# Optimization experiments

Measured on AMD Instinct MI355X. Metric: run time of the kernel, lower is better.

Reference implementation:

```python
import jax, jax.numpy as jnp
import numpy as np

N_NODES = 100000
N_EDGES = 1000000
NUM_FEATURES = 64
HIDDEN = 64
NUM_GRAPHS = 128


def setup_inputs() -> dict:
    key = jax.random.key(0)
    ks = jax.random.split(key, 12)
    x = jax.random.normal(ks[0], (N_NODES, NUM_FEATURES), dtype=jnp.float32)
    edge_index = jax.random.randint(ks[1], (2, N_EDGES), 0, N_NODES, dtype=jnp.int64)
    edge_weight = jax.random.uniform(ks[2], (N_EDGES,), dtype=jnp.float32)
    batch = jnp.sort(jax.random.randint(ks[3], (N_NODES,), 0, NUM_GRAPHS, dtype=jnp.int64))
    s1 = 1.0 / np.sqrt(NUM_FEATURES)
    s2 = 1.0 / np.sqrt(HIDDEN)
    # GraphConv layer 1: lin_rel (with bias) applied to aggregated msgs, lin_root (no bias)
    w1_rel = jax.random.uniform(ks[4], (HIDDEN, NUM_FEATURES), jnp.float32, -s1, s1)
    b1_rel = jax.random.uniform(ks[5], (HIDDEN,), jnp.float32, -s1, s1)
    w1_root = jax.random.uniform(ks[6], (HIDDEN, NUM_FEATURES), jnp.float32, -s1, s1)
    # GraphConv layer 2
    w2_rel = jax.random.uniform(ks[7], (HIDDEN, HIDDEN), jnp.float32, -s2, s2)
    b2_rel = jax.random.uniform(ks[8], (HIDDEN,), jnp.float32, -s2, s2)
    w2_root = jax.random.uniform(ks[9], (HIDDEN, HIDDEN), jnp.float32, -s2, s2)
    # final Linear(hidden, 1)
    w_lin = jax.random.uniform(ks[10], (1, HIDDEN), jnp.float32, -s2, s2)
    b_lin = jax.random.uniform(ks[11], (1,), jnp.float32, -s2, s2)
    return {
        "x": x, "edge_index": edge_index, "edge_weight": edge_weight, "batch": batch,
        "w1_rel": w1_rel, "b1_rel": b1_rel, "w1_root": w1_root,
        "w2_rel": w2_rel, "b2_rel": b2_rel, "w2_root": w2_root,
        "w_lin": w_lin, "b_lin": b_lin,
    }


def graph_conv(x, edge_index, edge_weight, w_rel, b_rel, w_root):
    # messages: x[src] * e, scatter-add into dst  (gather-scale-scatter)
    src, dst = edge_index[0], edge_index[1]
    msgs = x[src] * edge_weight[:, None]                      # [E, F]
    aggr = jax.ops.segment_sum(msgs, dst, num_segments=x.shape[0])  # [N, F]
    return aggr @ w_rel.T + b_rel + x @ w_root.T


def reference(x, edge_index, edge_weight, batch,
              w1_rel, b1_rel, w1_root, w2_rel, b2_rel, w2_root, w_lin, b_lin):
    h = graph_conv(x, edge_index, edge_weight, w1_rel, b1_rel, w1_root)
    h = jax.nn.relu(h)
    h = graph_conv(h, edge_index, edge_weight, w2_rel, b2_rel, w2_root)
    # global_mean_pool over graph ids
    sums = jax.ops.segment_sum(h, batch, num_segments=NUM_GRAPHS)          # [G, H]
    counts = jax.ops.segment_sum(jnp.ones((h.shape[0],), h.dtype), batch,
                                 num_segments=NUM_GRAPHS)                  # [G]
    pooled = sums / jnp.maximum(counts, 1.0)[:, None]
    # dropout(p=0.5) in eval mode is identity
    return pooled @ w_lin.T + b_lin                                        # [G, 1]
```

## Files before the change

kernel.cpp:

```cpp
#include <hip/hip_runtime.h>
#include <hip/hip_bf16.h>


#define N_NODES 100000
#define N_EDGES 1000000
#define NGRAPHS 128
#define BN 512
#define NBUCK ((N_NODES + BN - 1) / BN)
#define FILL_T 16
#define FILL_TILE (256 * FILL_T)
#define FILL_NB ((N_EDGES + FILL_TILE - 1) / FILL_TILE)
#define NTILES (N_NODES / 16)
#define AST 72

#define PREP_CVT_NB 3125
#define HIST0 (PREP_CVT_NB + 1)
#define HIST_NB 256
#define CNT0 (HIST0 + HIST_NB)
#define CNT_NB 64
#define PREP_TOTAL (CNT0 + CNT_NB)

typedef __attribute__((ext_vector_type(8))) short bf16x8;
typedef __attribute__((ext_vector_type(8))) unsigned short u16x8;
typedef __attribute__((ext_vector_type(4))) float f32x4;
typedef __attribute__((ext_vector_type(2))) float f32x2;

__device__ __forceinline__ unsigned short f2bf(float f) {
    unsigned u = __float_as_uint(f);
    unsigned r = (u + 0x7FFFu + ((u >> 16) & 1u)) >> 16;
    return (unsigned short)r;
}
__device__ __forceinline__ float bf2f(unsigned short h) {
    return __uint_as_float(((unsigned)h) << 16);
}
__device__ __forceinline__ void fma4(int w, float wt, float* a) {
    f32x2 lo = __builtin_amdgcn_cvt_pk_f32_fp8(w, false);
    f32x2 hi = __builtin_amdgcn_cvt_pk_f32_fp8(w, true);
    a[0] += wt * lo[0];
    a[1] += wt * lo[1];
    a[2] += wt * hi[0];
    a[3] += wt * hi[1];
}
__device__ __forceinline__ int pack4(float f0, float f1, float f2, float f3) {
    int w = __builtin_amdgcn_cvt_pk_fp8_f32(f0, f1, 0, false);
    w = __builtin_amdgcn_cvt_pk_fp8_f32(f2, f3, w, true);
    return w;
}
__device__ __forceinline__ bf16x8 fp8_to_bf16x8(int2 rx) {
    f32x2 a0 = __builtin_amdgcn_cvt_pk_f32_fp8(rx.x, false);
    f32x2 a1 = __builtin_amdgcn_cvt_pk_f32_fp8(rx.x, true);
    f32x2 a2 = __builtin_amdgcn_cvt_pk_f32_fp8(rx.y, false);
    f32x2 a3 = __builtin_amdgcn_cvt_pk_f32_fp8(rx.y, true);
    bf16x8 o;
    o[0] = (short)f2bf(a0[0]); o[1] = (short)f2bf(a0[1]);
    o[2] = (short)f2bf(a1[0]); o[3] = (short)f2bf(a1[1]);
    o[4] = (short)f2bf(a2[0]); o[5] = (short)f2bf(a2[1]);
    o[6] = (short)f2bf(a3[0]); o[7] = (short)f2bf(a3[1]);
    return o;
}

__global__ __launch_bounds__(256) void prep_all_kernel(
    const float* __restrict__ x, int* __restrict__ xf8,
    const float* __restrict__ w1rel, const float* __restrict__ w1root,
    const float* __restrict__ w2rel, const float* __restrict__ w2root,
    const float* __restrict__ wlin, const float* __restrict__ b2rel,
    const float* __restrict__ blin, unsigned short* __restrict__ whirel,
    unsigned short* __restrict__ wlorel, unsigned short* __restrict__ whiroot,
    unsigned short* __restrict__ wloroot, float* __restrict__ u,
    float* __restrict__ v, float* __restrict__ C,
    const int* __restrict__ ei, int* __restrict__ bcount,
    const int* __restrict__ batch, float* __restrict__ gc, int E) {
    int tid = threadIdx.x;
    if (blockIdx.x < PREP_CVT_NB) {
        int i = blockIdx.x * 256 + tid;
        const float4* xp = (const float4*)x + (size_t)i * 2;
        float4 a = xp[0], b = xp[1];
        int2 o8;
        o8.x = pack4(a.x, a.y, a.z, a.w);
        o8.y = pack4(b.x, b.y, b.z, b.w);
        *((int2*)xf8 + i) = o8;
        return;
    }
    if (blockIdx.x == PREP_CVT_NB) {
        for (int k = tid; k < 4096; k += 256) {
            float a = w1rel[k];
            unsigned short hi = f2bf(a);
            whirel[k] = hi;
            wlorel[k] = f2bf(a - bf2f(hi));
            float b = w1root[k];
            unsigned short hb = f2bf(b);
            whiroot[k] = hb;
            wloroot[k] = f2bf(b - bf2f(hb));
        }
        if (tid < 64) {
            float uu = 0.f, vv = 0.f;
            for (int h = 0; h < 64; ++h) {
                float wl = wlin[h];
                uu += wl * w2rel[h * 64 + tid];
                vv += wl * w2root[h * 64 + tid];
            }
            u[tid] = uu;
            v[tid] = vv;
        }
        if (tid == 0) {
            float c = blin[0];
            for (int h = 0; h < 64; ++h) c += wlin[h] * b2rel[h];
            *C = c;
        }
        return;
    }
    if (blockIdx.x < CNT0) {
        __shared__ int lh[NBUCK];
        for (int i = tid; i < NBUCK; i += 256) lh[i] = 0;
        __syncthreads();
        int hb = blockIdx.x - HIST0;
        for (int e = hb * 256 + tid; e < E; e += HIST_NB * 256)
            atomicAdd(&lh[ei[E + e] >> 9], 1);
        __syncthreads();
        for (int i = tid; i < NBUCK; i += 256) {
            int c = lh[i];
            if (c) atomicAdd(&bcount[i], c);
        }
        return;
    }
    {
        __shared__ int lgc[NGRAPHS];
        for (int i = tid; i < NGRAPHS; i += 256) lgc[i] = 0;
        __syncthreads();
        int cb = blockIdx.x - CNT0;
        for (int i = cb * 256 + tid; i < N_NODES; i += CNT_NB * 256)
            atomicAdd(&lgc[batch[i]], 1);
        __syncthreads();
        for (int i = tid; i < NGRAPHS; i += 256) {
            int c = lgc[i];
            if (c) atomicAdd(&gc[i], (float)c);
        }
    }
}

__global__ __launch_bounds__(256) void bucket_fill(
    const int* __restrict__ ei, const float* __restrict__ ew,
    const int* __restrict__ bcount, int* __restrict__ cursor,
    int2* __restrict__ ebuf, int E) {
    __shared__ int lh[NBUCK];
    __shared__ int gbase[NBUCK];
    __shared__ int sc[256];
    __shared__ int lbo[NBUCK];
    int tid = threadIdx.x;
    for (int i = tid; i < NBUCK; i += 256) lh[i] = 0;
    int v = (tid < NBUCK) ? bcount[tid] : 0;
    sc[tid] = v;
    __syncthreads();
    for (int off = 1; off < 256; off <<= 1) {
        int x = (tid >= off) ? sc[tid - off] : 0;
        __syncthreads();
        sc[tid] += x;
        __syncthreads();
    }
    if (tid < NBUCK) lbo[tid] = sc[tid] - v;
    __syncthreads();
    int base = blockIdx.x * FILL_TILE;
    int2 rec[FILL_T];
    int meta[FILL_T];
#pragma unroll
    for (int i = 0; i < FILL_T; ++i) {
        int e = base + i * 256 + tid;
        meta[i] = -1;
        if (e < E) {
            int src = ei[e];
            int dst = ei[E + e];
            int b = dst >> 9;
            int r = atomicAdd(&lh[b], 1);
            rec[i].x = src | ((dst & (BN - 1)) << 17);
            rec[i].y = __float_as_int(ew[e]);
            meta[i] = (b << 13) | r;
        }
    }
    __syncthreads();
    for (int i = tid; i < NBUCK; i += 256) {
        int c = lh[i];
        gbase[i] = c ? (lbo[i] + atomicAdd(&cursor[i], c)) : 0;
    }
    __syncthreads();
#pragma unroll
    for (int i = 0; i < FILL_T; ++i) {
        if (meta[i] >= 0) {
            int b = meta[i] >> 13;
            int r = meta[i] & 8191;
            ebuf[gbase[b] + r] = rec[i];
        }
    }
}

__global__ __launch_bounds__(512) void csr_build(
    const int* __restrict__ bcount, const int2* __restrict__ ebuf,
    const int* __restrict__ batch, int* __restrict__ row_ptr,
    int2* __restrict__ csr, int N) {
    __shared__ int s[BN];
    int b = blockIdx.x;
    int t = threadIdx.x;
    int vv = (t < NBUCK) ? bcount[t] : 0;
    if (t < 256) s[t] = vv;
    __syncthreads();
    for (int off = 1; off < 256; off <<= 1) {
        int x = (t >= off && t < 256) ? s[t - off] : 0;
        __syncthreads();
        if (t < 256) s[t] += x;
        __syncthreads();
    }
    int beg = (b == 0) ? 0 : s[b - 1];
    int end = s[b];
    __syncthreads();
    s[t] = 0;
    __syncthreads();
    for (int j = beg + t; j < end; j += 512)
        atomicAdd(&s[(ebuf[j].x >> 17) & (BN - 1)], 1);
    __syncthreads();
    int v = s[t];
    for (int off = 1; off < BN; off <<= 1) {
        int x = (t >= off) ? s[t - off] : 0;
        __syncthreads();
        s[t] += x;
        __syncthreads();
    }
    int excl = s[t] - v;
    int gidx = b * BN + t;
    if (gidx <= N) row_ptr[gidx] = beg + excl;
    __syncthreads();
    s[t] = excl;
    __syncthreads();
    for (int j = beg + t; j < end; j += 512) {
        int2 rec = ebuf[j];
        int dlo = (rec.x >> 17) & (BN - 1);
        int g = batch[b * BN + dlo];
        int r = atomicAdd(&s[dlo], 1);
        int2 o;
        o.x = (rec.x & 0x1FFFF) | (g << 17);
        o.y = rec.y;
        csr[beg + r] = o;
    }
}

__global__ __launch_bounds__(256) void gather_dense_kernel(
    const unsigned char* __restrict__ xf8,
    const int* __restrict__ row_ptr, const int2* __restrict__ csr,
    const unsigned short* __restrict__ whirel,
    const unsigned short* __restrict__ wlorel,
    const unsigned short* __restrict__ whiroot,
    const unsigned short* __restrict__ wloroot,
    const float* __restrict__ b1rel, const float* __restrict__ u,
    const float* __restrict__ v, float* __restrict__ p, float* __restrict__ q,
    int ntiles) {
    __shared__ unsigned short arow[4][16 * AST];
    int lane = threadIdx.x & 63;
    int wv = threadIdx.x >> 6;
    int wave = (blockIdx.x << 2) + wv;
    if (wave >= ntiles) return;
    unsigned short* my = &arow[wv][0];
    int nb = wave * 16;

    {
        int g4 = lane >> 2;
        int c4 = lane & 3;
        int node = nb + g4;
        int beg = row_ptr[node], end = row_ptr[node + 1];
        float a[16];
#pragma unroll
        for (int t = 0; t < 16; ++t) a[t] = 0.f;
        const unsigned char* xb = xf8 + (size_t)c4 * 16;
        for (int j = beg; j < end; j += 4) {
            int i1 = (j + 1 < end) ? j + 1 : j;
            int i2 = (j + 2 < end) ? j + 2 : j;
            int i3 = (j + 3 < end) ? j + 3 : j;
            int2 e0 = csr[j];
            int2 e1 = csr[i1];
            int2 e2 = csr[i2];
            int2 e3 = csr[i3];
            int4 r0 = *(const int4*)(xb + (size_t)(e0.x & 0x1FFFF) * 64);
            int4 r1 = *(const int4*)(xb + (size_t)(e1.x & 0x1FFFF) * 64);
            int4 r2 = *(const int4*)(xb + (size_t)(e2.x & 0x1FFFF) * 64);
            int4 r3 = *(const int4*)(xb + (size_t)(e3.x & 0x1FFFF) * 64);
            float w0 = __int_as_float(e0.y);
            float w1 = (j + 1 < end) ? __int_as_float(e1.y) : 0.f;
            float w2 = (j + 2 < end) ? __int_as_float(e2.y) : 0.f;
            float w3 = (j + 3 < end) ? __int_as_float(e3.y) : 0.f;
            fma4(r0.x, w0, a + 0);
            fma4(r0.y, w0, a + 4);
            fma4(r0.z, w0, a + 8);
            fma4(r0.w, w0, a + 12);
            fma4(r1.x, w1, a + 0);
            fma4(r1.y, w1, a + 4);
            fma4(r1.z, w1, a + 8);
            fma4(r1.w, w1, a + 12);
            fma4(r2.x, w2, a + 0);
            fma4(r2.y, w2, a + 4);
            fma4(r2.z, w2, a + 8);
            fma4(r2.w, w2, a + 12);
            fma4(r3.x, w3, a + 0);
            fma4(r3.y, w3, a + 4);
            fma4(r3.z, w3, a + 8);
            fma4(r3.w, w3, a + 12);
        }
        u16x8 o0, o1;
#pragma unroll
        for (int t = 0; t < 8; ++t) {
            o0[t] = f2bf(a[t]);
            o1[t] = f2bf(a[8 + t]);
        }
        *(u16x8*)(my + g4 * AST + c4 * 16) = o0;
        *(u16x8*)(my + g4 * AST + c4 * 16 + 8) = o1;
    }

    int lo4 = lane & 15;
    int quad = lane >> 4;
    f32x4 acc4[4];
#pragma unroll
    for (int t = 0; t < 4; ++t) acc4[t] = (f32x4){0.f, 0.f, 0.f, 0.f};
#pragma unroll
    for (int s = 0; s < 2; ++s) {
        bf16x8 Aa = *(const bf16x8*)(my + lo4 * AST + s * 32 + quad * 8);
        int2 rx = *(const int2*)(xf8 + (size_t)(nb + lo4) * 64 + s * 32 +
                                 quad * 8);
        bf16x8 Ax = fp8_to_bf16x8(rx);
#pragma unroll
        for (int t = 0; t < 4; ++t) {
            int off = (t * 16 + lo4) * 64 + s * 32 + quad * 8;
            bf16x8 bhr = *(const bf16x8*)(whirel + off);
            bf16x8 blr = *(const bf16x8*)(wlorel + off);
            bf16x8 bhx = *(const bf16x8*)(whiroot + off);
            bf16x8 blx = *(const bf16x8*)(wloroot + off);
            acc4[t] = __builtin_amdgcn_mfma_f32_16x16x32_bf16(Aa, bhr, acc4[t],
                                                              0, 0, 0);
            acc4[t] = __builtin_amdgcn_mfma_f32_16x16x32_bf16(Aa, blr, acc4[t],
                                                              0, 0, 0);
            acc4[t] = __builtin_amdgcn_mfma_f32_16x16x32_bf16(Ax, bhx, acc4[t],
                                                              0, 0, 0);
            acc4[t] = __builtin_amdgcn_mfma_f32_16x16x32_bf16(Ax, blx, acc4[t],
                                                              0, 0, 0);
        }
    }

    float pc[4] = {0.f, 0.f, 0.f, 0.f};
    float qc[4] = {0.f, 0.f, 0.f, 0.f};
#pragma unroll
    for (int t = 0; t < 4; ++t) {
        float bb = b1rel[t * 16 + lo4];
        float uu = u[t * 16 + lo4];
        float vv = v[t * 16 + lo4];
#pragma unroll
        for (int r = 0; r < 4; ++r) {
            float h1 = fmaxf(acc4[t][r] + bb, 0.f);
            pc[r] += uu * h1;
            qc[r] += vv * h1;
        }
    }
#pragma unroll
    for (int off = 1; off < 16; off <<= 1) {
#pragma unroll
        for (int r = 0; r < 4; ++r) {
            pc[r] += __shfl_xor(pc[r], off);
            qc[r] += __shfl_xor(qc[r], off);
        }
    }
    if (lo4 == 0) {
        f32x4 po = {pc[0], pc[1], pc[2], pc[3]};
        f32x4 qo = {qc[0], qc[1], qc[2], qc[3]};
        *(f32x4*)(p + nb + quad * 4) = po;
        *(f32x4*)(q + nb + quad * 4) = qo;
    }
}

#define PT_EPT 8
#define PT_EPW (64 * PT_EPT)
#define PT_NB ((N_EDGES + 4 * PT_EPW - 1) / (4 * PT_EPW))
#define PS_NB 98
__global__ __launch_bounds__(256) void pool_both(
    const int2* __restrict__ csr, const float* __restrict__ p,
    const float* __restrict__ q, const int* __restrict__ batch,
    float* __restrict__ gp, float* __restrict__ gq,
    const float* __restrict__ gc, int* __restrict__ done,
    const float* __restrict__ C, float* __restrict__ out, int E, int N) {
    __shared__ float lbuf[NGRAPHS];
    __shared__ int amLast;
    int tid = threadIdx.x;
    if (tid < NGRAPHS) lbuf[tid] = 0.f;
    __syncthreads();
    if (blockIdx.x < PT_NB) {
        int lane = tid & 63;
        int wid = (blockIdx.x * 256 + tid) >> 6;
        int base = wid * PT_EPW;
        float acc = 0.f;
        int curg = -1;
#pragma unroll
        for (int i = 0; i < PT_EPT; ++i) {
            int j = base + i * 64 + lane;
            if (j < E) {
                int2 e = csr[j];
                int g = ((unsigned)e.x) >> 17;
                float val = __int_as_float(e.y) * p[e.x & 0x1FFFF];
                if (g != curg) {
                    if (curg >= 0) atomicAdd(&lbuf[curg], acc);
                    curg = g;
                    acc = 0.f;
                }
                acc += val;
            }
        }
        if (curg >= 0) atomicAdd(&lbuf[curg], acc);
        __syncthreads();
        if (tid < NGRAPHS) {
            float t = lbuf[tid];
            if (t != 0.f) atomicAdd(&gp[tid], t);
        }
    } else {
        int bid = blockIdx.x - PT_NB;
        for (int i = bid * 256 + tid; i < N; i += PS_NB * 256) {
            atomicAdd(&lbuf[batch[i]], q[i]);
        }
        __syncthreads();
        if (tid < NGRAPHS) {
            float t = lbuf[tid];
            if (t != 0.f) atomicAdd(&gq[tid], t);
        }
    }
    __syncthreads();
    if (tid == 0) {
        __threadfence();
        amLast = (atomicAdd(done, 1) == PT_NB + PS_NB - 1);
    }
    __syncthreads();
    if (amLast) {
        __threadfence();
        if (tid < NGRAPHS) {
            float pv = atomicAdd(&gp[tid], 0.f);
            float qv = atomicAdd(&gq[tid], 0.f);
            float cv = atomicAdd((float*)&gc[tid], 0.f);
            out[tid] = (pv + qv) / fmaxf(cv, 1.f) + C[0];
        }
    }
}

extern "C" void kernel_launch(void* const* d_in, const int* in_sizes, int n_in,
                              void* d_out, int out_size, void* d_ws,
                              size_t ws_size, hipStream_t stream) {
    const float* x      = (const float*)d_in[0];
    const int*   ei     = (const int*)d_in[1];
    const float* ew     = (const float*)d_in[2];
    const int*   batch  = (const int*)d_in[3];
    const float* w1rel  = (const float*)d_in[4];
    const float* b1rel  = (const float*)d_in[5];
    const float* w1root = (const float*)d_in[6];
    const float* w2rel  = (const float*)d_in[7];
    const float* b2rel  = (const float*)d_in[8];
    const float* w2root = (const float*)d_in[9];
    const float* wlin   = (const float*)d_in[10];
    const float* blin   = (const float*)d_in[11];
    float* out = (float*)d_out;

    char* wsb = (char*)d_ws;
    int2* csr  = (int2*)wsb;
    int2* ebuf = (int2*)(wsb + (size_t)N_EDGES * 8);
    char* tail = wsb + (size_t)N_EDGES * 16;
    unsigned short* whirel  = (unsigned short*)tail;
    unsigned short* wlorel  = whirel + 4096;
    unsigned short* whiroot = wlorel + 4096;
    unsigned short* wloroot = whiroot + 4096;
    float* p  = (float*)(wloroot + 4096);
    float* q  = p + N_NODES;
    float* u  = q + N_NODES;
    float* v  = u + 64;
    float* C  = v + 64;
    int*   bcount = (int*)(C + 1);
    float* gp = (float*)(bcount + NBUCK);
    float* gq = gp + NGRAPHS;
    float* gc = gq + NGRAPHS;
    int*   done   = (int*)(gc + NGRAPHS);
    int*   cursor = done + 1;
    int*   row_ptr = cursor + NBUCK;
    int*   xf8 = (int*)(row_ptr + N_NODES + 2);

    hipMemsetAsync(bcount, 0, (2 * NBUCK + 3 * NGRAPHS + 1) * sizeof(int),
                   stream);

    prep_all_kernel<<<PREP_TOTAL, 256, 0, stream>>>(
        x, xf8, w1rel, w1root, w2rel, w2root, wlin, b2rel, blin, whirel,
        wlorel, whiroot, wloroot, u, v, C, ei, bcount, batch, gc, N_EDGES);

    bucket_fill<<<FILL_NB, 256, 0, stream>>>(ei, ew, bcount, cursor, ebuf,
                                             N_EDGES);
    csr_build<<<NBUCK, 512, 0, stream>>>(bcount, ebuf, batch, row_ptr, csr,
                                         N_NODES);

    gather_dense_kernel<<<(NTILES + 3) / 4, 256, 0, stream>>>(
        (const unsigned char*)xf8, row_ptr, csr, whirel, wlorel, whiroot,
        wloroot, b1rel, u, v, p, q, NTILES);

    pool_both<<<PT_NB + PS_NB, 256, 0, stream>>>(csr, p, q, batch, gp, gq, gc,
                                                 done, C, out, N_EDGES,
                                                 N_NODES);
}
```

Baseline: 205.4 us.

## Fuse CSR build with gather-dense layer and drop memset via per-block histograms

Merges the per-bucket CSR construction and the first-layer gather plus MFMA transform into one kernel, so each 256-node bucket sorts its edges and then aggregates them while the row pointers stay in shared memory. The global row_ptr array is no longer needed. The edge histogram now writes per-block partial counts instead of global atomics, and graph sizes come from binary search over the sorted batch array. Together these remove the hipMemsetAsync and the separate counting blocks. In exchange, every consumer block must re-sum 64 partial histograms, bucket size is halved to 256 nodes, and the gather now depends on the CSR writes made in the same block being visible to its own reads.

```diff
diff --git a/kernel.cpp b/kernel.cpp
--- a/kernel.cpp
+++ b/kernel.cpp
@@ -5,20 +5,17 @@
 #define N_NODES 100000
 #define N_EDGES 1000000
 #define NGRAPHS 128
-#define BN 512
+#define BN 256
 #define NBUCK ((N_NODES + BN - 1) / BN)
 #define FILL_T 16
 #define FILL_TILE (256 * FILL_T)
 #define FILL_NB ((N_EDGES + FILL_TILE - 1) / FILL_TILE)
-#define NTILES (N_NODES / 16)
 #define AST 72
 
 #define PREP_CVT_NB 3125
 #define HIST0 (PREP_CVT_NB + 1)
-#define HIST_NB 256
-#define CNT0 (HIST0 + HIST_NB)
-#define CNT_NB 64
-#define PREP_TOTAL (CNT0 + CNT_NB)
+#define HIST_NB 64
+#define PREP_TOTAL (HIST0 + HIST_NB)
 
 typedef __attribute__((ext_vector_type(8))) short bf16x8;
 typedef __attribute__((ext_vector_type(8))) unsigned short u16x8;
@@ -68,8 +65,9 @@
     unsigned short* __restrict__ wlorel, unsigned short* __restrict__ whiroot,
     unsigned short* __restrict__ wloroot, float* __restrict__ u,
     float* __restrict__ v, float* __restrict__ C,
-    const int* __restrict__ ei, int* __restrict__ bcount,
-    const int* __restrict__ batch, float* __restrict__ gc, int E) {
+    const int* __restrict__ ei, int* __restrict__ bpart,
+    const int* __restrict__ batch, float* __restrict__ gc,
+    int* __restrict__ cursor, int E) {
     int tid = threadIdx.x;
     if (blockIdx.x < PREP_CVT_NB) {
         int i = blockIdx.x * 256 + tid;
@@ -107,69 +105,75 @@
             for (int h = 0; h < 64; ++h) c += wlin[h] * b2rel[h];
             *C = c;
         }
+        if (tid < NGRAPHS) {
+            int g = tid;
+            int lo = 0, hi = N_NODES;
+            while (lo < hi) {
+                int m = (lo + hi) >> 1;
+                if (batch[m] < g) lo = m + 1; else hi = m;
+            }
+            int lo2 = lo, hi2 = N_NODES;
+            while (lo2 < hi2) {
+                int m = (lo2 + hi2) >> 1;
+                if (batch[m] < g + 1) lo2 = m + 1; else hi2 = m;
+            }
+            gc[g] = (float)(lo2 - lo);
+        }
+        for (int i = tid; i < NBUCK; i += 256) cursor[i] = 0;
         return;
     }
-    if (blockIdx.x < CNT0) {
+    {
         __shared__ int lh[NBUCK];
         for (int i = tid; i < NBUCK; i += 256) lh[i] = 0;
         __syncthreads();
         int hb = blockIdx.x - HIST0;
         for (int e = hb * 256 + tid; e < E; e += HIST_NB * 256)
-            atomicAdd(&lh[ei[E + e] >> 9], 1);
-        __syncthreads();
-        for (int i = tid; i < NBUCK; i += 256) {
-            int c = lh[i];
-            if (c) atomicAdd(&bcount[i], c);
-        }
-        return;
-    }
-    {
-        __shared__ int lgc[NGRAPHS];
-        for (int i = tid; i < NGRAPHS; i += 256) lgc[i] = 0;
-        __syncthreads();
-        int cb = blockIdx.x - CNT0;
-        for (int i = cb * 256 + tid; i < N_NODES; i += CNT_NB * 256)
-            atomicAdd(&lgc[batch[i]], 1);
-        __syncthreads();
-        for (int i = tid; i < NGRAPHS; i += 256) {
-            int c = lgc[i];
-            if (c) atomicAdd(&gc[i], (float)c);
-        }
+            atomicAdd(&lh[ei[E + e] >> 8], 1);
+        __syncthreads();
+        for (int i = tid; i < NBUCK; i += 256) bpart[hb * NBUCK + i] = lh[i];
     }
 }
 
 __global__ __launch_bounds__(256) void bucket_fill(
     const int* __restrict__ ei, const float* __restrict__ ew,
-    const int* __restrict__ bcount, int* __restrict__ cursor,
+    const int* __restrict__ bpart, int* __restrict__ cursor,
     int2* __restrict__ ebuf, int E) {
     __shared__ int lh[NBUCK];
     __shared__ int gbase[NBUCK];
-    __shared__ int sc[256];
     __shared__ int lbo[NBUCK];
-    int tid = threadIdx.x;
-    for (int i = tid; i < NBUCK; i += 256) lh[i] = 0;
-    int v = (tid < NBUCK) ? bcount[tid] : 0;
-    sc[tid] = v;
-    __syncthreads();
-    for (int off = 1; off < 256; off <<= 1) {
-        int x = (tid >= off) ? sc[tid - off] : 0;
-        __syncthreads();
-        sc[tid] += x;
-        __syncthreads();
-    }
-    if (tid < NBUCK) lbo[tid] = sc[tid] - v;
+    __shared__ int sc_[512];
+    int t = threadIdx.x;
+    for (int i = t; i < NBUCK; i += 256) lh[i] = 0;
+    int b0 = 0, b1 = 0;
+    if (t < NBUCK)
+        for (int h = 0; h < HIST_NB; ++h) b0 += bpart[h * NBUCK + t];
+    if (t + 256 < NBUCK)
+        for (int h = 0; h < HIST_NB; ++h) b1 += bpart[h * NBUCK + t + 256];
+    sc_[t] = (t < NBUCK) ? b0 : 0;
+    sc_[t + 256] = (t + 256 < NBUCK) ? b1 : 0;
+    __syncthreads();
+    for (int off = 1; off < 512; off <<= 1) {
+        int a0 = (t >= off) ? sc_[t - off] : 0;
+        int a1 = ((t + 256) >= off) ? sc_[t + 256 - off] : 0;
+        __syncthreads();
+        sc_[t] += a0;
+        sc_[t + 256] += a1;
+        __syncthreads();
+    }
+    if (t < NBUCK) lbo[t] = sc_[t] - b0;
+    if (t + 256 < NBUCK) lbo[t + 256] = sc_[t + 256] - b1;
     __syncthreads();
     int base = blockIdx.x * FILL_TILE;
     int2 rec[FILL_T];
     int meta[FILL_T];
 #pragma unroll
     for (int i = 0; i < FILL_T; ++i) {
-        int e = base + i * 256 + tid;
+        int e = base + i * 256 + t;
         meta[i] = -1;
         if (e < E) {
             int src = ei[e];
             int dst = ei[E + e];
-            int b = dst >> 9;
+            int b = dst >> 8;
             int r = atomicAdd(&lh[b], 1);
             rec[i].x = src | ((dst & (BN - 1)) << 17);
             rec[i].y = __float_as_int(ew[e]);
@@ -177,7 +181,7 @@
         }
     }
     __syncthreads();
-    for (int i = tid; i < NBUCK; i += 256) {
+    for (int i = t; i < NBUCK; i += 256) {
         int c = lh[i];
         gbase[i] = c ? (lbo[i] + atomicAdd(&cursor[i], c)) : 0;
     }
@@ -192,181 +196,187 @@
     }
 }
 
-__global__ __launch_bounds__(512) void csr_build(
-    const int* __restrict__ bcount, const int2* __restrict__ ebuf,
-    const int* __restrict__ batch, int* __restrict__ row_ptr,
-    int2* __restrict__ csr, int N) {
-    __shared__ int s[BN];
-    int b = blockIdx.x;
-    int t = threadIdx.x;
-    int vv = (t < NBUCK) ? bcount[t] : 0;
-    if (t < 256) s[t] = vv;
-    __syncthreads();
-    for (int off = 1; off < 256; off <<= 1) {
-        int x = (t >= off && t < 256) ? s[t - off] : 0;
-        __syncthreads();
-        if (t < 256) s[t] += x;
-        __syncthreads();
-    }
-    int beg = (b == 0) ? 0 : s[b - 1];
-    int end = s[b];
-    __syncthreads();
-    s[t] = 0;
-    __syncthreads();
-    for (int j = beg + t; j < end; j += 512)
-        atomicAdd(&s[(ebuf[j].x >> 17) & (BN - 1)], 1);
-    __syncthreads();
-    int v = s[t];
-    for (int off = 1; off < BN; off <<= 1) {
-        int x = (t >= off) ? s[t - off] : 0;
-        __syncthreads();
-        s[t] += x;
-        __syncthreads();
-    }
-    int excl = s[t] - v;
-    int gidx = b * BN + t;
-    if (gidx <= N) row_ptr[gidx] = beg + excl;
-    __syncthreads();
-    s[t] = excl;
-    __syncthreads();
-    for (int j = beg + t; j < end; j += 512) {
-        int2 rec = ebuf[j];
-        int dlo = (rec.x >> 17) & (BN - 1);
-        int g = batch[b * BN + dlo];
-        int r = atomicAdd(&s[dlo], 1);
-        int2 o;
-        o.x = (rec.x & 0x1FFFF) | (g << 17);
-        o.y = rec.y;
-        csr[beg + r] = o;
-    }
-}
-
-__global__ __launch_bounds__(256) void gather_dense_kernel(
+__global__ __launch_bounds__(512) void csr_gather_kernel(
+    const int2* __restrict__ ebuf, const int* __restrict__ bpart,
+    const int* __restrict__ batch, int2* __restrict__ csr,
     const unsigned char* __restrict__ xf8,
-    const int* __restrict__ row_ptr, const int2* __restrict__ csr,
     const unsigned short* __restrict__ whirel,
     const unsigned short* __restrict__ wlorel,
     const unsigned short* __restrict__ whiroot,
     const unsigned short* __restrict__ wloroot,
     const float* __restrict__ b1rel, const float* __restrict__ u,
     const float* __restrict__ v, float* __restrict__ p, float* __restrict__ q,
-    int ntiles) {
-    __shared__ unsigned short arow[4][16 * AST];
-    int lane = threadIdx.x & 63;
-    int wv = threadIdx.x >> 6;
-    int wave = (blockIdx.x << 2) + wv;
-    if (wave >= ntiles) return;
-    unsigned short* my = &arow[wv][0];
-    int nb = wave * 16;
-
-    {
-        int g4 = lane >> 2;
-        int c4 = lane & 3;
-        int node = nb + g4;
-        int beg = row_ptr[node], end = row_ptr[node + 1];
-        float a[16];
-#pragma unroll
-        for (int t = 0; t < 16; ++t) a[t] = 0.f;
-        const unsigned char* xb = xf8 + (size_t)c4 * 16;
-        for (int j = beg; j < end; j += 4) {
-            int i1 = (j + 1 < end) ? j + 1 : j;
-            int i2 = (j + 2 < end) ? j + 2 : j;
-            int i3 = (j + 3 < end) ? j + 3 : j;
-            int2 e0 = csr[j];
-            int2 e1 = csr[i1];
-            int2 e2 = csr[i2];
-            int2 e3 = csr[i3];
-            int4 r0 = *(const int4*)(xb + (size_t)(e0.x & 0x1FFFF) * 64);
-            int4 r1 = *(const int4*)(xb + (size_t)(e1.x & 0x1FFFF) * 64);
-            int4 r2 = *(const int4*)(xb + (size_t)(e2.x & 0x1FFFF) * 64);
-            int4 r3 = *(const int4*)(xb + (size_t)(e3.x & 0x1FFFF) * 64);
-            float w0 = __int_as_float(e0.y);
-            float w1 = (j + 1 < end) ? __int_as_float(e1.y) : 0.f;
-            float w2 = (j + 2 < end) ? __int_as_float(e2.y) : 0.f;
-            float w3 = (j + 3 < end) ? __int_as_float(e3.y) : 0.f;
-            fma4(r0.x, w0, a + 0);
-            fma4(r0.y, w0, a + 4);
-            fma4(r0.z, w0, a + 8);
-            fma4(r0.w, w0, a + 12);
-            fma4(r1.x, w1, a + 0);
-            fma4(r1.y, w1, a + 4);
-            fma4(r1.z, w1, a + 8);
-            fma4(r1.w, w1, a + 12);
-            fma4(r2.x, w2, a + 0);
-            fma4(r2.y, w2, a + 4);
-            fma4(r2.z, w2, a + 8);
-            fma4(r2.w, w2, a + 12);
-            fma4(r3.x, w3, a + 0);
-            fma4(r3.y, w3, a + 4);
-            fma4(r3.z, w3, a + 8);
-            fma4(r3.w, w3, a + 12);
-        }
-        u16x8 o0, o1;
-#pragma unroll
-        for (int t = 0; t < 8; ++t) {
-            o0[t] = f2bf(a[t]);
-            o1[t] = f2bf(a[8 + t]);
-        }
-        *(u16x8*)(my + g4 * AST + c4 * 16) = o0;
-        *(u16x8*)(my + g4 * AST + c4 * 16 + 8) = o1;
-    }
-
-    int lo4 = lane & 15;
-    int quad = lane >> 4;
-    f32x4 acc4[4];
-#pragma unroll
-    for (int t = 0; t < 4; ++t) acc4[t] = (f32x4){0.f, 0.f, 0.f, 0.f};
-#pragma unroll
-    for (int s = 0; s < 2; ++s) {
-        bf16x8 Aa = *(const bf16x8*)(my + lo4 * AST + s * 32 + quad * 8);
-        int2 rx = *(const int2*)(xf8 + (size_t)(nb + lo4) * 64 + s * 32 +
-                                 quad * 8);
-        bf16x8 Ax = fp8_to_bf16x8(rx);
-#pragma unroll
-        for (int t = 0; t < 4; ++t) {
-            int off = (t * 16 + lo4) * 64 + s * 32 + quad * 8;
-            bf16x8 bhr = *(const bf16x8*)(whirel + off);
-            bf16x8 blr = *(const bf16x8*)(wlorel + off);
-            bf16x8 bhx = *(const bf16x8*)(whiroot + off);
-            bf16x8 blx = *(const bf16x8*)(wloroot + off);
-            acc4[t] = __builtin_amdgcn_mfma_f32_16x16x32_bf16(Aa, bhr, acc4[t],
-                                                              0, 0, 0);
-            acc4[t] = __builtin_amdgcn_mfma_f32_16x16x32_bf16(Aa, blr, acc4[t],
-                                                              0, 0, 0);
-            acc4[t] = __builtin_amdgcn_mfma_f32_16x16x32_bf16(Ax, bhx, acc4[t],
-                                                              0, 0, 0);
-            acc4[t] = __builtin_amdgcn_mfma_f32_16x16x32_bf16(Ax, blx, acc4[t],
-                                                              0, 0, 0);
-        }
-    }
-
-    float pc[4] = {0.f, 0.f, 0.f, 0.f};
-    float qc[4] = {0.f, 0.f, 0.f, 0.f};
-#pragma unroll
-    for (int t = 0; t < 4; ++t) {
-        float bb = b1rel[t * 16 + lo4];
-        float uu = u[t * 16 + lo4];
-        float vv = v[t * 16 + lo4];
-#pragma unroll
-        for (int r = 0; r < 4; ++r) {
-            float h1 = fmaxf(acc4[t][r] + bb, 0.f);
-            pc[r] += uu * h1;
-            qc[r] += vv * h1;
-        }
-    }
-#pragma unroll
-    for (int off = 1; off < 16; off <<= 1) {
-#pragma unroll
-        for (int r = 0; r < 4; ++r) {
-            pc[r] += __shfl_xor(pc[r], off);
-            qc[r] += __shfl_xor(qc[r], off);
-        }
-    }
-    if (lo4 == 0) {
-        f32x4 po = {pc[0], pc[1], pc[2], pc[3]};
-        f32x4 qo = {qc[0], qc[1], qc[2], qc[3]};
-        *(f32x4*)(p + nb + quad * 4) = po;
-        *(f32x4*)(q + nb + quad * 4) = qo;
+    float* __restrict__ gp, float* __restrict__ gq, int* __restrict__ done) {
+    __shared__ int sc_[512];
+    __shared__ int deg[BN];
+    __shared__ int rp[BN + 1];
+    __shared__ int cur[BN];
+    __shared__ unsigned short arow[8][16 * AST];
+    int t = threadIdx.x;
+    int b = blockIdx.x;
+    if (b == 0) {
+        if (t < NGRAPHS) { gp[t] = 0.f; gq[t] = 0.f; }
+        if (t == NGRAPHS) *done = 0;
+    }
+    int bc = 0;
+    if (t < NBUCK)
+        for (int h = 0; h < HIST_NB; ++h) bc += bpart[h * NBUCK + t];
+    sc_[t] = (t < NBUCK) ? bc : 0;
+    __syncthreads();
+    for (int off = 1; off < 512; off <<= 1) {
+        int xv = (t >= off) ? sc_[t - off] : 0;
+        __syncthreads();
+        sc_[t] += xv;
+        __syncthreads();
+    }
+    int beg = (b == 0) ? 0 : sc_[b - 1];
+    int end = sc_[b];
+    __syncthreads();
+    if (t < BN) deg[t] = 0;
+    __syncthreads();
+    for (int j = beg + t; j < end; j += 512)
+        atomicAdd(&deg[(ebuf[j].x >> 17) & (BN - 1)], 1);
+    __syncthreads();
+    if (t < BN) sc_[t] = deg[t];
+    __syncthreads();
+    for (int off = 1; off < BN; off <<= 1) {
+        int xv = 0;
+        if (t < BN && t >= off) xv = sc_[t - off];
+        __syncthreads();
+        if (t < BN) sc_[t] += xv;
+        __syncthreads();
+    }
+    if (t < BN) {
+        int r0 = beg + sc_[t] - deg[t];
+        rp[t] = r0;
+        cur[t] = r0;
+    }
+    if (t == 0) rp[BN] = end;
+    __syncthreads();
+    for (int j = beg + t; j < end; j += 512) {
+        int2 rec = ebuf[j];
+        int dlo = (rec.x >> 17) & (BN - 1);
+        int g = batch[b * BN + dlo];
+        int r = atomicAdd(&cur[dlo], 1);
+        int2 o;
+        o.x = (rec.x & 0x1FFFF) | (g << 17);
+        o.y = rec.y;
+        csr[r] = o;
+    }
+    __syncthreads();
+    int lane = t & 63;
+    int w = t >> 6;
+    unsigned short* my = &arow[w][0];
+    for (int tt = w; tt < 16; tt += 8) {
+        int nb = b * BN + tt * 16;
+        if (nb >= N_NODES) continue;
+        {
+            int g4 = lane >> 2;
+            int c4 = lane & 3;
+            int nrel = tt * 16 + g4;
+            int ebeg = rp[nrel], eend = rp[nrel + 1];
+            float a[16];
+#pragma unroll
+            for (int k = 0; k < 16; ++k) a[k] = 0.f;
+            const unsigned char* xb = xf8 + (size_t)c4 * 16;
+            for (int j = ebeg; j < eend; j += 4) {
+                int i1 = (j + 1 < eend) ? j + 1 : j;
+                int i2 = (j + 2 < eend) ? j + 2 : j;
+                int i3 = (j + 3 < eend) ? j + 3 : j;
+                int2 e0 = csr[j];
+                int2 e1 = csr[i1];
+                int2 e2 = csr[i2];
+                int2 e3 = csr[i3];
+                int4 r0 = *(const int4*)(xb + (size_t)(e0.x & 0x1FFFF) * 64);
+                int4 r1 = *(const int4*)(xb + (size_t)(e1.x & 0x1FFFF) * 64);
+                int4 r2 = *(const int4*)(xb + (size_t)(e2.x & 0x1FFFF) * 64);
+                int4 r3 = *(const int4*)(xb + (size_t)(e3.x & 0x1FFFF) * 64);
+                float w0 = __int_as_float(e0.y);
+                float w1 = (j + 1 < eend) ? __int_as_float(e1.y) : 0.f;
+                float w2 = (j + 2 < eend) ? __int_as_float(e2.y) : 0.f;
+                float w3 = (j + 3 < eend) ? __int_as_float(e3.y) : 0.f;
+                fma4(r0.x, w0, a + 0);
+                fma4(r0.y, w0, a + 4);
+                fma4(r0.z, w0, a + 8);
+                fma4(r0.w, w0, a + 12);
+                fma4(r1.x, w1, a + 0);
+                fma4(r1.y, w1, a + 4);
+                fma4(r1.z, w1, a + 8);
+                fma4(r1.w, w1, a + 12);
+                fma4(r2.x, w2, a + 0);
+                fma4(r2.y, w2, a + 4);
+                fma4(r2.z, w2, a + 8);
+                fma4(r2.w, w2, a + 12);
+                fma4(r3.x, w3, a + 0);
+                fma4(r3.y, w3, a + 4);
+                fma4(r3.z, w3, a + 8);
+                fma4(r3.w, w3, a + 12);
+            }
+            u16x8 o0, o1;
+#pragma unroll
+            for (int k = 0; k < 8; ++k) {
+                o0[k] = f2bf(a[k]);
+                o1[k] = f2bf(a[8 + k]);
+            }
+            *(u16x8*)(my + g4 * AST + c4 * 16) = o0;
+            *(u16x8*)(my + g4 * AST + c4 * 16 + 8) = o1;
+        }
+        int lo4 = lane & 15;
+        int quad = lane >> 4;
+        f32x4 acc4[4];
+#pragma unroll
+        for (int k = 0; k < 4; ++k) acc4[k] = (f32x4){0.f, 0.f, 0.f, 0.f};
+#pragma unroll
+        for (int s = 0; s < 2; ++s) {
+            bf16x8 Aa = *(const bf16x8*)(my + lo4 * AST + s * 32 + quad * 8);
+            int2 rx = *(const int2*)(xf8 + (size_t)(nb + lo4) * 64 + s * 32 +
+                                     quad * 8);
+            bf16x8 Ax = fp8_to_bf16x8(rx);
+#pragma unroll
+            for (int k = 0; k < 4; ++k) {
+                int off = (k * 16 + lo4) * 64 + s * 32 + quad * 8;
+                bf16x8 bhr = *(const bf16x8*)(whirel + off);
+                bf16x8 blr = *(const bf16x8*)(wlorel + off);
+                bf16x8 bhx = *(const bf16x8*)(whiroot + off);
+                bf16x8 blx = *(const bf16x8*)(wloroot + off);
+                acc4[k] = __builtin_amdgcn_mfma_f32_16x16x32_bf16(
+                    Aa, bhr, acc4[k], 0, 0, 0);
+                acc4[k] = __builtin_amdgcn_mfma_f32_16x16x32_bf16(
+                    Aa, blr, acc4[k], 0, 0, 0);
+                acc4[k] = __builtin_amdgcn_mfma_f32_16x16x32_bf16(
+                    Ax, bhx, acc4[k], 0, 0, 0);
+                acc4[k] = __builtin_amdgcn_mfma_f32_16x16x32_bf16(
+                    Ax, blx, acc4[k], 0, 0, 0);
+            }
+        }
+        float pc[4] = {0.f, 0.f, 0.f, 0.f};
+        float qc[4] = {0.f, 0.f, 0.f, 0.f};
+#pragma unroll
+        for (int k = 0; k < 4; ++k) {
+            float bb = b1rel[k * 16 + lo4];
+            float uu = u[k * 16 + lo4];
+            float vv = v[k * 16 + lo4];
+#pragma unroll
+            for (int r = 0; r < 4; ++r) {
+                float h1 = fmaxf(acc4[k][r] + bb, 0.f);
+                pc[r] += uu * h1;
+                qc[r] += vv * h1;
+            }
+        }
+#pragma unroll
+        for (int off = 1; off < 16; off <<= 1) {
+#pragma unroll
+            for (int r = 0; r < 4; ++r) {
+                pc[r] += __shfl_xor(pc[r], off);
+                qc[r] += __shfl_xor(qc[r], off);
+            }
+        }
+        if (lo4 == 0) {
+            f32x4 po = {pc[0], pc[1], pc[2], pc[3]};
+            f32x4 qo = {qc[0], qc[1], qc[2], qc[3]};
+            *(f32x4*)(p + nb + quad * 4) = po;
+            *(f32x4*)(q + nb + quad * 4) = qo;
+        }
     }
 }
 
@@ -461,7 +471,8 @@
     int2* csr  = (int2*)wsb;
     int2* ebuf = (int2*)(wsb + (size_t)N_EDGES * 8);
     char* tail = wsb + (size_t)N_EDGES * 16;
-    unsigned short* whirel  = (unsigned short*)tail;
+    int* xf8 = (int*)tail;
+    unsigned short* whirel  = (unsigned short*)(tail + (size_t)N_NODES * 64);
     unsigned short* wlorel  = whirel + 4096;
     unsigned short* whiroot = wlorel + 4096;
     unsigned short* wloroot = whiroot + 4096;
@@ -470,30 +481,24 @@
     float* u  = q + N_NODES;
     float* v  = u + 64;
     float* C  = v + 64;
-    int*   bcount = (int*)(C + 1);
-    float* gp = (float*)(bcount + NBUCK);
+    float* gp = C + 1;
     float* gq = gp + NGRAPHS;
     float* gc = gq + NGRAPHS;
     int*   done   = (int*)(gc + NGRAPHS);
     int*   cursor = done + 1;
-    int*   row_ptr = cursor + NBUCK;
-    int*   xf8 = (int*)(row_ptr + N_NODES + 2);
-
-    hipMemsetAsync(bcount, 0, (2 * NBUCK + 3 * NGRAPHS + 1) * sizeof(int),
-                   stream);
+    int*   bpart  = cursor + NBUCK;
 
     prep_all_kernel<<<PREP_TOTAL, 256, 0, stream>>>(
         x, xf8, w1rel, w1root, w2rel, w2root, wlin, b2rel, blin, whirel,
-        wlorel, whiroot, wloroot, u, v, C, ei, bcount, batch, gc, N_EDGES);
-
-    bucket_fill<<<FILL_NB, 256, 0, stream>>>(ei, ew, bcount, cursor, ebuf,
+        wlorel, whiroot, wloroot, u, v, C, ei, bpart, batch, gc, cursor,
+        N_EDGES);
+
+    bucket_fill<<<FILL_NB, 256, 0, stream>>>(ei, ew, bpart, cursor, ebuf,
                                              N_EDGES);
-    csr_build<<<NBUCK, 512, 0, stream>>>(bcount, ebuf, batch, row_ptr, csr,
-                                         N_NODES);
-
-    gather_dense_kernel<<<(NTILES + 3) / 4, 256, 0, stream>>>(
-        (const unsigned char*)xf8, row_ptr, csr, whirel, wlorel, whiroot,
-        wloroot, b1rel, u, v, p, q, NTILES);
+
+    csr_gather_kernel<<<NBUCK, 512, 0, stream>>>(
+        ebuf, bpart, batch, csr, (const unsigned char*)xf8, whirel, wlorel,
+        whiroot, wloroot, b1rel, u, v, p, q, gp, gq, done);
 
     pool_both<<<PT_NB + PS_NB, 256, 0, stream>>>(csr, p, q, batch, gp, gq, gc,
                                                  done, C, out, N_EDGES,
```

After: 212.2 us. +3.3%, slower.

## Drop memset launch by using per-block histogram partials and binary-search graph counts

Applied to the files above, without the earlier changes.

Removes the hipMemsetAsync launch. Each histogram block now writes its bucket counts to its own slot in a partials array, and consumers sum those slots instead of relying on global atomics into a zeroed buffer. Graph node counts come from a binary search over the sorted batch array, replacing the atomic counting blocks. Cursors and the pooling accumulators are zeroed inside the earlier kernels. In exchange, every bucket_fill and csr_build block re-sums 64 partials per bucket, adding redundant reads.

```diff
diff --git a/kernel.cpp b/kernel.cpp
--- a/kernel.cpp
+++ b/kernel.cpp
@@ -15,10 +15,8 @@
 
 #define PREP_CVT_NB 3125
 #define HIST0 (PREP_CVT_NB + 1)
-#define HIST_NB 256
-#define CNT0 (HIST0 + HIST_NB)
-#define CNT_NB 64
-#define PREP_TOTAL (CNT0 + CNT_NB)
+#define HIST_NB 64
+#define PREP_TOTAL (HIST0 + HIST_NB)
 
 typedef __attribute__((ext_vector_type(8))) short bf16x8;
 typedef __attribute__((ext_vector_type(8))) unsigned short u16x8;
@@ -68,8 +66,9 @@
     unsigned short* __restrict__ wlorel, unsigned short* __restrict__ whiroot,
     unsigned short* __restrict__ wloroot, float* __restrict__ u,
     float* __restrict__ v, float* __restrict__ C,
-    const int* __restrict__ ei, int* __restrict__ bcount,
-    const int* __restrict__ batch, float* __restrict__ gc, int E) {
+    const int* __restrict__ ei, int* __restrict__ bpart,
+    const int* __restrict__ batch, float* __restrict__ gc,
+    int* __restrict__ cursor, int E) {
     int tid = threadIdx.x;
     if (blockIdx.x < PREP_CVT_NB) {
         int i = blockIdx.x * 256 + tid;
@@ -107,9 +106,24 @@
             for (int h = 0; h < 64; ++h) c += wlin[h] * b2rel[h];
             *C = c;
         }
+        if (tid < NGRAPHS) {
+            int g = tid;
+            int lo = 0, hi = N_NODES;
+            while (lo < hi) {
+                int m = (lo + hi) >> 1;
+                if (batch[m] < g) lo = m + 1; else hi = m;
+            }
+            int lo2 = lo, hi2 = N_NODES;
+            while (lo2 < hi2) {
+                int m = (lo2 + hi2) >> 1;
+                if (batch[m] < g + 1) lo2 = m + 1; else hi2 = m;
+            }
+            gc[g] = (float)(lo2 - lo);
+        }
+        for (int i = tid; i < NBUCK; i += 256) cursor[i] = 0;
         return;
     }
-    if (blockIdx.x < CNT0) {
+    {
         __shared__ int lh[NBUCK];
         for (int i = tid; i < NBUCK; i += 256) lh[i] = 0;
         __syncthreads();
@@ -117,30 +131,13 @@
         for (int e = hb * 256 + tid; e < E; e += HIST_NB * 256)
             atomicAdd(&lh[ei[E + e] >> 9], 1);
         __syncthreads();
-        for (int i = tid; i < NBUCK; i += 256) {
-            int c = lh[i];
-            if (c) atomicAdd(&bcount[i], c);
-        }
-        return;
-    }
-    {
-        __shared__ int lgc[NGRAPHS];
-        for (int i = tid; i < NGRAPHS; i += 256) lgc[i] = 0;
-        __syncthreads();
-        int cb = blockIdx.x - CNT0;
-        for (int i = cb * 256 + tid; i < N_NODES; i += CNT_NB * 256)
-            atomicAdd(&lgc[batch[i]], 1);
-        __syncthreads();
-        for (int i = tid; i < NGRAPHS; i += 256) {
-            int c = lgc[i];
-            if (c) atomicAdd(&gc[i], (float)c);
-        }
+        for (int i = tid; i < NBUCK; i += 256) bpart[hb * NBUCK + i] = lh[i];
     }
 }
 
 __global__ __launch_bounds__(256) void bucket_fill(
     const int* __restrict__ ei, const float* __restrict__ ew,
-    const int* __restrict__ bcount, int* __restrict__ cursor,
+    const int* __restrict__ bpart, int* __restrict__ cursor,
     int2* __restrict__ ebuf, int E) {
     __shared__ int lh[NBUCK];
     __shared__ int gbase[NBUCK];
@@ -148,8 +145,10 @@
     __shared__ int lbo[NBUCK];
     int tid = threadIdx.x;
     for (int i = tid; i < NBUCK; i += 256) lh[i] = 0;
-    int v = (tid < NBUCK) ? bcount[tid] : 0;
-    sc[tid] = v;
+    int v = 0;
+    if (tid < NBUCK)
+        for (int h = 0; h < HIST_NB; ++h) v += bpart[h * NBUCK + tid];
+    sc[tid] = (tid < NBUCK) ? v : 0;
     __syncthreads();
     for (int off = 1; off < 256; off <<= 1) {
         int x = (tid >= off) ? sc[tid - off] : 0;
@@ -193,14 +192,21 @@
 }
 
 __global__ __launch_bounds__(512) void csr_build(
-    const int* __restrict__ bcount, const int2* __restrict__ ebuf,
+    const int* __restrict__ bpart, const int2* __restrict__ ebuf,
     const int* __restrict__ batch, int* __restrict__ row_ptr,
-    int2* __restrict__ csr, int N) {
+    int2* __restrict__ csr, float* __restrict__ gp, float* __restrict__ gq,
+    int* __restrict__ done, int N) {
     __shared__ int s[BN];
     int b = blockIdx.x;
     int t = threadIdx.x;
-    int vv = (t < NBUCK) ? bcount[t] : 0;
-    if (t < 256) s[t] = vv;
+    if (b == 0) {
+        if (t < NGRAPHS) { gp[t] = 0.f; gq[t] = 0.f; }
+        if (t == NGRAPHS) *done = 0;
+    }
+    int vv = 0;
+    if (t < NBUCK)
+        for (int h = 0; h < HIST_NB; ++h) vv += bpart[h * NBUCK + t];
+    if (t < 256) s[t] = (t < NBUCK) ? vv : 0;
     __syncthreads();
     for (int off = 1; off < 256; off <<= 1) {
         int x = (t >= off && t < 256) ? s[t - off] : 0;
@@ -461,7 +467,8 @@
     int2* csr  = (int2*)wsb;
     int2* ebuf = (int2*)(wsb + (size_t)N_EDGES * 8);
     char* tail = wsb + (size_t)N_EDGES * 16;
-    unsigned short* whirel  = (unsigned short*)tail;
+    int* xf8 = (int*)tail;
+    unsigned short* whirel  = (unsigned short*)(tail + (size_t)N_NODES * 64);
     unsigned short* wlorel  = whirel + 4096;
     unsigned short* whiroot = wlorel + 4096;
     unsigned short* wloroot = whiroot + 4096;
@@ -470,26 +477,24 @@
     float* u  = q + N_NODES;
     float* v  = u + 64;
     float* C  = v + 64;
-    int*   bcount = (int*)(C + 1);
-    float* gp = (float*)(bcount + NBUCK);
+    float* gp = C + 1;
     float* gq = gp + NGRAPHS;
     float* gc = gq + NGRAPHS;
     int*   done   = (int*)(gc + NGRAPHS);
     int*   cursor = done + 1;
-    int*   row_ptr = cursor + NBUCK;
-    int*   xf8 = (int*)(row_ptr + N_NODES + 2);
-
-    hipMemsetAsync(bcount, 0, (2 * NBUCK + 3 * NGRAPHS + 1) * sizeof(int),
-                   stream);
+    int*   bpart  = cursor + NBUCK;
+    int*   row_ptr = bpart + HIST_NB * NBUCK;
 
     prep_all_kernel<<<PREP_TOTAL, 256, 0, stream>>>(
         x, xf8, w1rel, w1root, w2rel, w2root, wlin, b2rel, blin, whirel,
-        wlorel, whiroot, wloroot, u, v, C, ei, bcount, batch, gc, N_EDGES);
-
-    bucket_fill<<<FILL_NB, 256, 0, stream>>>(ei, ew, bcount, cursor, ebuf,
+        wlorel, whiroot, wloroot, u, v, C, ei, bpart, batch, gc, cursor,
+        N_EDGES);
+
+    bucket_fill<<<FILL_NB, 256, 0, stream>>>(ei, ew, bpart, cursor, ebuf,
                                              N_EDGES);
-    csr_build<<<NBUCK, 512, 0, stream>>>(bcount, ebuf, batch, row_ptr, csr,
-                                         N_NODES);
+
+    csr_build<<<NBUCK, 512, 0, stream>>>(bpart, ebuf, batch, row_ptr, csr,
+                                         gp, gq, done, N_NODES);
 
     gather_dense_kernel<<<(NTILES + 3) / 4, 256, 0, stream>>>(
         (const unsigned char*)xf8, row_ptr, csr, whirel, wlorel, whiroot,
```

New measurement: 203.3 us (median of 2 runs). Within noise of the previous version (-1.0%).
